# Kernel optimization log

Hardware: AMD Instinct MI355X
Metric: run time of the kernel (lower is better)

The kernel has to match this reference:

```python
import jax, jax.numpy as jnp
import numpy as np

MODEL_DIM = 128
N_FRAMES = 128
N_SAMPLES = 2 ** 15
N_TABLES = 16
TABLE_SIZE = 512
STD = 0.01


def _mlp(x, w1, b1, w2, b2, w3, b3):
    h = jax.nn.leaky_relu(x @ w1 + b1, 0.2)
    h = jax.nn.leaky_relu(h @ w2 + b2, 0.2)
    return h @ w3 + b3


def _interp_linear(x, out_size):
    # x: (B, T_in) -> (B, out_size); torch F.interpolate(mode='linear', align_corners=False)
    t_in = x.shape[-1]
    pos = (jnp.arange(out_size, dtype=x.dtype) + 0.5) * (t_in / out_size) - 0.5
    pos = jnp.clip(pos, 0.0, t_in - 1.0)
    lo = jnp.floor(pos).astype(jnp.int32)
    hi = jnp.minimum(lo + 1, t_in - 1)
    w = pos - lo.astype(x.dtype)
    return x[:, lo] * (1.0 - w) + x[:, hi] * w


def setup_inputs() -> dict:
    key = jax.random.key(0)
    ks = jax.random.split(key, 11)

    def lin(k, i, o):
        kw, kb = jax.random.split(k)
        return (jax.random.normal(kw, (i, o), jnp.float32) * (0.1 / np.sqrt(i)),
                jax.random.normal(kb, (o,), jnp.float32) * 0.01)

    x = jax.random.normal(ks[0], (8, MODEL_DIM), jnp.float32)
    wavetables = jax.random.uniform(ks[1], (N_TABLES, TABLE_SIZE), jnp.float32, -1.0, 1.0)
    tc_w1, tc_b1 = lin(ks[2], MODEL_DIM, MODEL_DIM)
    tc_w2, tc_b2 = lin(ks[3], MODEL_DIM, MODEL_DIM)
    tc_w3, tc_b3 = lin(ks[4], MODEL_DIM, N_TABLES * 16)
    env_w1, env_b1 = lin(ks[5], MODEL_DIM, MODEL_DIM)
    env_w2, env_b2 = lin(ks[6], MODEL_DIM, MODEL_DIM)
    env_w3, env_b3 = lin(ks[7], MODEL_DIM, N_FRAMES)
    fr_w1, fr_b1 = lin(ks[8], MODEL_DIM, MODEL_DIM)
    fr_w2, fr_b2 = lin(ks[9], MODEL_DIM, MODEL_DIM)
    fr_w3, fr_b3 = lin(ks[10], MODEL_DIM, N_FRAMES)
    return dict(x=x, wavetables=wavetables,
                tc_w1=tc_w1, tc_b1=tc_b1, tc_w2=tc_w2, tc_b2=tc_b2, tc_w3=tc_w3, tc_b3=tc_b3,
                env_w1=env_w1, env_b1=env_b1, env_w2=env_w2, env_b2=env_b2, env_w3=env_w3, env_b3=env_b3,
                fr_w1=fr_w1, fr_b1=fr_b1, fr_w2=fr_w2, fr_b2=fr_b2, fr_w3=fr_w3, fr_b3=fr_b3)


def reference(x, wavetables,
              tc_w1, tc_b1, tc_w2, tc_b2, tc_w3, tc_b3,
              env_w1, env_b1, env_w2, env_b2, env_w3, env_b3,
              fr_w1, fr_b1, fr_w2, fr_b2, fr_w3, fr_b3):
    batch = x.shape[0]

    # table choice head -> per-item table selection (reconstructs `indices`/`values` in source)
    tc = _mlp(x, tc_w1, tc_b1, tc_w2, tc_b2, tc_w3, tc_b3).reshape(batch, N_TABLES, 16)
    scores = tc.mean(axis=-1)                       # (B, n_tables)
    indices = jnp.argmax(scores, axis=-1)           # (B,)
    values = jnp.max(scores, axis=-1)               # (B,)

    # normalized wavetables
    wt = wavetables / (jnp.max(wavetables, axis=-1, keepdims=True) + 1e-8)
    selected_tables = wt[indices][:, None, :]       # (B, 1, table_size)

    # amplitude envelope
    env = _mlp(x, env_w1, env_b1, env_w2, env_b2, env_w3, env_b3)  # (B, n_frames)
    env = _interp_linear(env ** 2, N_SAMPLES)       # (B, n_samples)

    # instantaneous frequency -> phase in [0, 1)
    freq = _mlp(x, fr_w1, fr_b1, fr_w2, fr_b2, fr_w3, fr_b3) ** 2  # (B, n_frames)
    freq = _interp_linear(freq, N_SAMPLES)          # (B, n_samples)
    phase = jnp.cumsum(freq, axis=-1) % 1.0         # (B, n_samples)

    # Gaussian pdf sampling kernel over table positions: (B, table_size, n_samples)
    grid = jnp.linspace(0.0, 1.0, TABLE_SIZE)
    z = (grid[None, :, None] - phase[:, None, :]) / STD
    kernel = jnp.exp(-0.5 * z * z) / (STD * np.sqrt(2.0 * np.pi))
    sampling_kernel = jnp.transpose(kernel, (0, 2, 1))  # (B, n_samples, table_size)

    # resample the selected table via batched matmul
    sampled = selected_tables @ kernel              # (B, 1, n_samples)
    sampled = sampled * env[:, None, :] * values[:, None, None]
    return sampled, sampling_kernel
```

## Files before the change

kernel.cpp:

```cpp
#include <hip/hip_runtime.h>
#include <hip/hip_bf16.h>
#include <math.h>

typedef __hip_bfloat16 bf16;
typedef float f32x4 __attribute__((ext_vector_type(4)));

#define BATCH    8
#define DIM      128
#define NFRAMES  128
#define NSAMP    32768
#define NTAB     16
#define TSIZE    512

__device__ __forceinline__ float ld(const void* p, int i, bool f32) {
    return f32 ? ((const float*)p)[i] : __bfloat162float(((const bf16*)p)[i]);
}

#define WS_VALUES 0
#define WS_ENV    64
#define WS_FREQ   1088
#define WS_SEL    2112
#define WS_PHASE  6208

__global__ __launch_bounds__(1024) void kA_prep(
    const void* __restrict__ x, const void* __restrict__ wav,
    const void* tw1, const void* tb1, const void* tw2, const void* tb2,
    const void* tw3, const void* tb3,
    const void* ew1, const void* eb1, const void* ew2, const void* eb2,
    const void* ew3, const void* eb3,
    const void* fw1, const void* fb1, const void* fw2, const void* fb2,
    const void* fw3, const void* fb3,
    float* __restrict__ ws)
{
    const int b   = blockIdx.x;
    const int tid = threadIdx.x;

    __shared__ int    s_isf32;
    __shared__ float  xs[DIM];
    __shared__ float  h1s[3][DIM];
    __shared__ float  h2s[3][DIM];
    __shared__ float  o3tc[256];
    __shared__ float  envf[NFRAMES];
    __shared__ float  frf[NFRAMES];
    __shared__ float  scores[16];
    __shared__ float  red[512];
    __shared__ int    s_idx;
    __shared__ double sums[1024];

    if (tid == 0) s_isf32 = 0;
    __syncthreads();
    {
        const unsigned short* xb = (const unsigned short*)x;
        if (tid < 1024) {
            const int e = (xb[tid] >> 7) & 0xFF;
            if (e >= 132) s_isf32 = 1;
        }
    }
    __syncthreads();
    const bool F32 = (s_isf32 != 0);

    if (tid < DIM) xs[tid] = ld(x, b*DIM + tid, F32);
    __syncthreads();

    const void* W1h[3] = {tw1, ew1, fw1};
    const void* B1h[3] = {tb1, eb1, fb1};
    const void* W2h[3] = {tw2, ew2, fw2};
    const void* B2h[3] = {tb2, eb2, fb2};

    if (tid < 384) {
        const int head = tid >> 7, o = tid & 127;
        double acc = (double)ld(B1h[head], o, F32);
        const void* W = W1h[head];
        for (int k = 0; k < DIM; k++)
            acc += (double)xs[k] * (double)ld(W, k*DIM + o, F32);
        float v = (float)acc;
        h1s[head][o] = v > 0.f ? v : 0.2f*v;
    }
    __syncthreads();

    if (tid < 384) {
        const int head = tid >> 7, o = tid & 127;
        double acc = (double)ld(B2h[head], o, F32);
        const void* W = W2h[head];
        const float* hh = h1s[head];
        for (int k = 0; k < DIM; k++)
            acc += (double)hh[k] * (double)ld(W, k*DIM + o, F32);
        float v = (float)acc;
        h2s[head][o] = v > 0.f ? v : 0.2f*v;
    }
    __syncthreads();

    if (tid < 256) {
        const int o = tid;
        double acc = (double)ld(tb3, o, F32);
        const float* hh = h2s[0];
        for (int k = 0; k < DIM; k++)
            acc += (double)hh[k] * (double)ld(tw3, k*256 + o, F32);
        o3tc[o] = (float)acc;
    } else if (tid < 384) {
        const int o = tid - 256;
        double acc = (double)ld(eb3, o, F32);
        const float* hh = h2s[1];
        for (int k = 0; k < DIM; k++)
            acc += (double)hh[k] * (double)ld(ew3, k*DIM + o, F32);
        const float v = (float)acc;
        envf[o] = v * v;
    } else if (tid < 512) {
        const int o = tid - 384;
        double acc = (double)ld(fb3, o, F32);
        const float* hh = h2s[2];
        for (int k = 0; k < DIM; k++)
            acc += (double)hh[k] * (double)ld(fw3, k*DIM + o, F32);
        const float v = (float)acc;
        frf[o] = v * v;
    }
    __syncthreads();

    if (tid < 16) {
        float s = 0.f;
        for (int j = 0; j < 16; j++) s += o3tc[tid*16 + j];
        scores[tid] = s * (1.0f/16.0f);
    }
    __syncthreads();
    if (tid == 0) {
        float best = scores[0]; int bi = 0;
        for (int i = 1; i < 16; i++)
            if (scores[i] > best) { best = scores[i]; bi = i; }
        s_idx = bi;
        ws[WS_VALUES + b] = best;
    }
    __syncthreads();

    const int idx = s_idx;
    float wv_t = 0.f;
    if (tid < 512) { wv_t = ld(wav, idx*TSIZE + tid, F32); red[tid] = wv_t; }
    __syncthreads();
    for (int off = 256; off; off >>= 1) {
        if (tid < off) red[tid] = fmaxf(red[tid], red[tid + off]);
        __syncthreads();
    }
    const float mx = red[0] + 1e-8f;
    if (tid < 512) ws[WS_SEL + b*TSIZE + tid] = wv_t / mx;
    if (tid < NFRAMES) ws[WS_ENV + b*NFRAMES + tid] = envf[tid];

    const int SPT = NSAMP / 1024;
    const int s0  = tid * SPT;
    double v[32];
    double local = 0.0;
    #pragma unroll
    for (int i = 0; i < SPT; i++) {
        const int s = s0 + i;
        double pos = ((double)s + 0.5) * (1.0/256.0) - 0.5;
        pos = fmin(fmax(pos, 0.0), 127.0);
        const int lo = (int)pos;
        int hi = lo + 1; if (hi > 127) hi = 127;
        const double w = pos - (double)lo;
        const double f = (double)frf[lo] * (1.0 - w) + (double)frf[hi] * w;
        v[i] = f;
        local += f;
    }
    sums[tid] = local;
    __syncthreads();
    for (int off = 1; off < 1024; off <<= 1) {
        const double add = (tid >= off) ? sums[tid - off] : 0.0;
        __syncthreads();
        sums[tid] += add;
        __syncthreads();
    }
    double run = sums[tid] - local;
    float* phase = ws + WS_PHASE + (size_t)b * NSAMP;
    #pragma unroll
    for (int i = 0; i < SPT; i++) {
        run += v[i];
        phase[s0 + i] = (float)(run - floor(run));
    }
}

__global__ __launch_bounds__(256) void kB_synth(const float* __restrict__ ws,
                                                float* __restrict__ out)
{
    const int lane = threadIdx.x & 63;
    const int w    = (blockIdx.x << 2) + (threadIdx.x >> 6);
    const int r0   = w << 2;
    const int b    = r0 >> 15;

    const float* tab = ws + WS_SEL + b*TSIZE;
    const f32x4 tv0 = *reinterpret_cast<const f32x4*>(tab + 4*lane);
    const f32x4 tv1 = *reinterpret_cast<const f32x4*>(tab + 4*lane + 256);
    const float  val  = ws[WS_VALUES + b];
    const float* envf = ws + WS_ENV + b*NFRAMES;
    float* kbase = out + (size_t)BATCH*NSAMP + ((size_t)r0 << 9);

    float samp[4];
    #pragma unroll
    for (int i = 0; i < 4; i++) {
        const int r = r0 + i;
        const int s = r & (NSAMP - 1);
        const float p = ws[WS_PHASE + r];

        float pos = ((float)s + 0.5f) * (1.0f/256.0f) - 0.5f;
        pos = fminf(fmaxf(pos, 0.0f), 127.0f);
        const int lo = (int)pos;
        int hi = lo + 1; if (hi > 127) hi = 127;
        const float wq = pos - (float)lo;
        const float env = envf[lo]*(1.0f - wq) + envf[hi]*wq;

        float dot = 0.f;
        #pragma unroll
        for (int j = 0; j < 2; j++) {
            const int t0 = 4*lane + 256*j;
            const f32x4 tv = j ? tv1 : tv0;
            f32x4 o4;
            #pragma unroll
            for (int k = 0; k < 4; k++) {
                const float g = (float)(t0 + k) * (1.0f/511.0f);
                const float z = (g - p) * 100.0f;
                const float e = __expf(-0.5f*z*z) * 39.89422804014327f;
                dot += e * tv[k];
                o4[k] = e;
            }
            __builtin_nontemporal_store(o4,
                reinterpret_cast<f32x4*>(kbase + (i << 9) + t0));
        }

        #pragma unroll
        for (int m = 32; m; m >>= 1) dot += __shfl_xor(dot, m, 64);
        samp[i] = dot * env * val;
    }

    if (lane == 0) {
        f32x4 s4; s4[0] = samp[0]; s4[1] = samp[1]; s4[2] = samp[2]; s4[3] = samp[3];
        *reinterpret_cast<f32x4*>(out + r0) = s4;
    }
}

extern "C" void kernel_launch(void* const* d_in, const int* in_sizes, int n_in,
                              void* d_out, int out_size, void* d_ws, size_t ws_size,
                              hipStream_t stream)
{
    float* ws  = (float*)d_ws;
    float* out = (float*)d_out;

    hipLaunchKernelGGL(kA_prep, dim3(BATCH), dim3(1024), 0, stream,
        d_in[0], d_in[1],
        d_in[2],  d_in[3],  d_in[4],  d_in[5],  d_in[6],  d_in[7],
        d_in[8],  d_in[9],  d_in[10], d_in[11], d_in[12], d_in[13],
        d_in[14], d_in[15], d_in[16], d_in[17], d_in[18], d_in[19],
        ws);

    hipLaunchKernelGGL(kB_synth, dim3((BATCH*NSAMP)/16), dim3(256), 0, stream,
        ws, out);
}
```

Measured before the change: 626.1 us.

## Compute phase analytically from per-frame prefix sums instead of a full scan

The prep kernel no longer interpolates and scans all 32768 samples per batch item. It stores 129 per-frame prefix sums in double, and the synth kernel rebuilds each sample's cumulative phase in closed form from the linear-interpolation segment (a quadratic in the in-segment index). This removes the 1024-thread double-precision scan and the phase buffer round trip. Each wave now handles 8 rows instead of 4, and the grid offsets are precomputed per lane. The risks are extra double-precision math per sample in the hot kernel and small phase differences from the changed summation order.

Result: no change. 619.9 us (-1.0%).

```diff
diff --git a/kernel.cpp b/kernel.cpp
--- a/kernel.cpp
+++ b/kernel.cpp
@@ -22,7 +22,7 @@
 #define WS_SEL    2112
 #define WS_PHASE  6208
 
-__global__ __launch_bounds__(1024) void kA_prep(
+__global__ __launch_bounds__(512) void kA_prep(
     const void* __restrict__ x, const void* __restrict__ wav,
     const void* tw1, const void* tb1, const void* tw2, const void* tb2,
     const void* tw3, const void* tb3,
@@ -45,16 +45,14 @@
     __shared__ float  scores[16];
     __shared__ float  red[512];
     __shared__ int    s_idx;
-    __shared__ double sums[1024];
 
     if (tid == 0) s_isf32 = 0;
     __syncthreads();
     {
         const unsigned short* xb = (const unsigned short*)x;
-        if (tid < 1024) {
-            const int e = (xb[tid] >> 7) & 0xFF;
-            if (e >= 132) s_isf32 = 1;
-        }
+        const int e0 = (xb[tid] >> 7) & 0xFF;
+        const int e1 = (xb[tid + 512] >> 7) & 0xFF;
+        if (e0 >= 132 || e1 >= 132) s_isf32 = 1;
     }
     __syncthreads();
     const bool F32 = (s_isf32 != 0);
@@ -141,38 +139,20 @@
     }
     const float mx = red[0] + 1e-8f;
     if (tid < 512) ws[WS_SEL + b*TSIZE + tid] = wv_t / mx;
-    if (tid < NFRAMES) ws[WS_ENV + b*NFRAMES + tid] = envf[tid];
-
-    const int SPT = NSAMP / 1024;
-    const int s0  = tid * SPT;
-    double v[32];
-    double local = 0.0;
-    #pragma unroll
-    for (int i = 0; i < SPT; i++) {
-        const int s = s0 + i;
-        double pos = ((double)s + 0.5) * (1.0/256.0) - 0.5;
-        pos = fmin(fmax(pos, 0.0), 127.0);
-        const int lo = (int)pos;
-        int hi = lo + 1; if (hi > 127) hi = 127;
-        const double w = pos - (double)lo;
-        const double f = (double)frf[lo] * (1.0 - w) + (double)frf[hi] * w;
-        v[i] = f;
-        local += f;
-    }
-    sums[tid] = local;
-    __syncthreads();
-    for (int off = 1; off < 1024; off <<= 1) {
-        const double add = (tid >= off) ? sums[tid - off] : 0.0;
-        __syncthreads();
-        sums[tid] += add;
-        __syncthreads();
-    }
-    double run = sums[tid] - local;
-    float* phase = ws + WS_PHASE + (size_t)b * NSAMP;
-    #pragma unroll
-    for (int i = 0; i < SPT; i++) {
-        run += v[i];
-        phase[s0 + i] = (float)(run - floor(run));
+    if (tid < NFRAMES) {
+        ws[WS_ENV  + b*NFRAMES + tid] = envf[tid];
+        ws[WS_FREQ + b*NFRAMES + tid] = frf[tid];
+    }
+    __syncthreads();
+
+    if (tid == 0) {
+        double* D = (double*)(ws + WS_PHASE) + (size_t)b * 129;
+        double run = 128.0 * (double)frf[0];
+        D[0] = run;
+        for (int m = 0; m < 127; m++) {
+            run += 128.0 * ((double)frf[m] + (double)frf[m+1]);
+            D[m+1] = run;
+        }
     }
 }
 
@@ -181,22 +161,47 @@
 {
     const int lane = threadIdx.x & 63;
     const int w    = (blockIdx.x << 2) + (threadIdx.x >> 6);
-    const int r0   = w << 2;
+    const int r0   = w << 3;
     const int b    = r0 >> 15;
 
     const float* tab = ws + WS_SEL + b*TSIZE;
     const f32x4 tv0 = *reinterpret_cast<const f32x4*>(tab + 4*lane);
     const f32x4 tv1 = *reinterpret_cast<const f32x4*>(tab + 4*lane + 256);
     const float  val  = ws[WS_VALUES + b];
-    const float* envf = ws + WS_ENV + b*NFRAMES;
+    const float* envf = ws + WS_ENV  + b*NFRAMES;
+    const float* frq  = ws + WS_FREQ + b*NFRAMES;
+    const double* D   = (const double*)(ws + WS_PHASE) + (size_t)b * 129;
+    const double f0   = (double)frq[0];
+    const double f127 = (double)frq[127];
     float* kbase = out + (size_t)BATCH*NSAMP + ((size_t)r0 << 9);
 
-    float samp[4];
+    const float KS = 100.0f / 511.0f;
+    float zb0[4], zb1[4];
     #pragma unroll
-    for (int i = 0; i < 4; i++) {
+    for (int k = 0; k < 4; k++) {
+        zb0[k] = (float)(4*lane + k)       * KS;
+        zb1[k] = (float)(4*lane + 256 + k) * KS;
+    }
+
+    float samp[8];
+    #pragma unroll
+    for (int i = 0; i < 8; i++) {
         const int r = r0 + i;
         const int s = r & (NSAMP - 1);
-        const float p = ws[WS_PHASE + r];
+
+        double run;
+        if (s < 128) {
+            run = (double)(s + 1) * f0;
+        } else if (s >= 32640) {
+            run = D[127] + (double)(s - 32639) * f127;
+        } else {
+            const int m = (s - 128) >> 8;
+            const int n = ((s - 128) & 255) + 1;
+            const double a  = (double)frq[m];
+            const double bb = (double)frq[m + 1];
+            run = D[m] + (double)n * a + (bb - a) * ((double)(n * n) * (1.0 / 512.0));
+        }
+        const float poff = (float)(-100.0 * (run - floor(run)));
 
         float pos = ((float)s + 0.5f) * (1.0f/256.0f) - 0.5f;
         pos = fminf(fmaxf(pos, 0.0f), 127.0f);
@@ -213,8 +218,7 @@
             f32x4 o4;
             #pragma unroll
             for (int k = 0; k < 4; k++) {
-                const float g = (float)(t0 + k) * (1.0f/511.0f);
-                const float z = (g - p) * 100.0f;
+                const float z = (j ? zb1[k] : zb0[k]) + poff;
                 const float e = __expf(-0.5f*z*z) * 39.89422804014327f;
                 dot += e * tv[k];
                 o4[k] = e;
@@ -224,13 +228,16 @@
         }
 
         #pragma unroll
-        for (int m = 32; m; m >>= 1) dot += __shfl_xor(dot, m, 64);
+        for (int m2 = 32; m2; m2 >>= 1) dot += __shfl_xor(dot, m2, 64);
         samp[i] = dot * env * val;
     }
 
     if (lane == 0) {
-        f32x4 s4; s4[0] = samp[0]; s4[1] = samp[1]; s4[2] = samp[2]; s4[3] = samp[3];
-        *reinterpret_cast<f32x4*>(out + r0) = s4;
+        f32x4 a4, b4;
+        #pragma unroll
+        for (int k = 0; k < 4; k++) { a4[k] = samp[k]; b4[k] = samp[4+k]; }
+        *reinterpret_cast<f32x4*>(out + r0)     = a4;
+        *reinterpret_cast<f32x4*>(out + r0 + 4) = b4;
     }
 }
 
@@ -241,13 +248,13 @@
     float* ws  = (float*)d_ws;
     float* out = (float*)d_out;
 
-    hipLaunchKernelGGL(kA_prep, dim3(BATCH), dim3(1024), 0, stream,
+    hipLaunchKernelGGL(kA_prep, dim3(BATCH), dim3(512), 0, stream,
         d_in[0], d_in[1],
         d_in[2],  d_in[3],  d_in[4],  d_in[5],  d_in[6],  d_in[7],
         d_in[8],  d_in[9],  d_in[10], d_in[11], d_in[12], d_in[13],
         d_in[14], d_in[15], d_in[16], d_in[17], d_in[18], d_in[19],
         ws);
 
-    hipLaunchKernelGGL(kB_synth, dim3((BATCH*NSAMP)/16), dim3(256), 0, stream,
+    hipLaunchKernelGGL(kB_synth, dim3((BATCH*NSAMP)/32), dim3(256), 0, stream,
         ws, out);
 }
```
